# Kernel optimization log

Hardware: AMD Instinct MI355X
Metric: run time of the kernel (lower is better)

## Reference

```python
import jax, jax.numpy as jnp
import numpy as np
from jax import lax

B, T, V = 1024, 256, 64  # batch, time, num_classes (blank = V-1)
NEG = jnp.float32(-1e30)


def _greedy_decode(logits):
    """tf.nn.ctc_greedy_decoder: per-step argmax, merge repeated, drop blanks.
    Returns dense labels [B, T] (padded with blank) and lengths [B]."""
    blank = V - 1
    preds = jnp.argmax(logits, axis=-1).astype(jnp.int32)  # [B, T]
    prev = jnp.concatenate([jnp.full((B, 1), -1, jnp.int32), preds[:, :-1]], axis=1)
    keep = (preds != blank) & (preds != prev)  # merge_repeated=True
    pos = jnp.cumsum(keep, axis=1) - 1                      # target column for kept tokens
    col = jnp.where(keep, pos, T)                           # dump non-kept into scratch col T
    lab = jnp.full((B, T + 1), blank, jnp.int32)
    lab = lab.at[jnp.arange(B)[:, None], col].set(preds)[:, :T]
    length = jnp.sum(keep, axis=1).astype(jnp.int32)
    return lab, length


def _ctc_loss(logits, labels, lengths):
    """tf.nn.ctc_loss (blank_index=-1): log-space forward DP over extended labels."""
    blank = V - 1
    S = 2 * T + 1
    logp = jax.nn.log_softmax(logits)                       # [B, T, V]
    # extended label seq: blank, l1, blank, l2, ..., blank
    ext = jnp.full((B, S), blank, jnp.int32).at[:, 1::2].set(labels)
    ext_m2 = jnp.concatenate([jnp.full((B, 2), blank, jnp.int32), ext[:, :-2]], axis=1)
    allow_skip = (ext != blank) & (ext != ext_m2)           # [B, S]

    alpha0 = jnp.full((B, S), NEG, jnp.float32).at[:, 0].set(0.0)

    def step(alpha, logp_t):
        lp = jnp.take_along_axis(logp_t, ext, axis=1)       # [B, S]
        a2 = jnp.concatenate([jnp.full((B, 1), NEG), alpha[:, :-1]], axis=1)
        a3 = jnp.concatenate([jnp.full((B, 2), NEG), alpha[:, :-2]], axis=1)
        a3 = jnp.where(allow_skip, a3, NEG)
        new = jnp.logaddexp(jnp.logaddexp(alpha, a2), a3) + lp
        return new, None

    alpha, _ = lax.scan(step, alpha0, jnp.swapaxes(logp, 0, 1))  # scan over T
    end = 2 * lengths                                        # [B] index of final blank
    e1 = jnp.take_along_axis(alpha, end[:, None], axis=1)[:, 0]
    e2 = jnp.take_along_axis(alpha, jnp.maximum(end - 1, 0)[:, None], axis=1)[:, 0]
    e2 = jnp.where(lengths > 0, e2, NEG)
    return -jnp.logaddexp(e1, e2)


def setup_inputs() -> dict:
    key = jax.random.key(0)
    inputs = jax.random.normal(key, (B, T, V), dtype=jnp.float32)
    return {"inputs": inputs}


def reference(inputs):
    labels, lengths = _greedy_decode(inputs)
    loss = _ctc_loss(inputs, labels, lengths)
    probability = jnp.exp(-loss)
    # (decoded label ids stand in for the joined strings; lengths delimit them)
    return labels, lengths, probability
```

## Files before the change

kernel.cpp:

```cpp
#include <hip/hip_runtime.h>


#define BB 1024
#define TT 256
#define VV 64
#define BLANKC 63
#define K_LOG2E 1.44269504088896340736f

__global__ __launch_bounds__(256) void k1_decode(const float* __restrict__ logits,
                                                 float2* __restrict__ lsepb,
                                                 unsigned char* __restrict__ pred)
{
    const int gid = blockIdx.x * 256 + threadIdx.x;
    const float4* rp = (const float4*)(logits + (size_t)gid * VV);
    float4 v[16];
    #pragma unroll
    for (int i = 0; i < 16; ++i) v[i] = rp[i];

    float m = v[0].x; int idx = 0;
    #pragma unroll
    for (int i = 0; i < 16; ++i) {
        if (v[i].x > m) { m = v[i].x; idx = 4*i+0; }
        if (v[i].y > m) { m = v[i].y; idx = 4*i+1; }
        if (v[i].z > m) { m = v[i].z; idx = 4*i+2; }
        if (v[i].w > m) { m = v[i].w; idx = 4*i+3; }
    }
    float s0=0.f, s1=0.f, s2=0.f, s3=0.f;
    #pragma unroll
    for (int i = 0; i < 16; ++i) {
        s0 += exp2f((v[i].x - m) * K_LOG2E);
        s1 += exp2f((v[i].y - m) * K_LOG2E);
        s2 += exp2f((v[i].z - m) * K_LOG2E);
        s3 += exp2f((v[i].w - m) * K_LOG2E);
    }
    const float s = (s0 + s1) + (s2 + s3);
    const float lse2 = m * K_LOG2E + log2f(s);
    const float pb   = exp2f(fmaf(v[15].w, K_LOG2E, -lse2));
    lsepb[gid] = make_float2(lse2, pb);
    pred[gid]  = (unsigned char)idx;
}

#define STEP(XV, LS) { \
    const float lse2 = (LS).x, pbv = (LS).y; \
    const float q0 = exp2f(fmaf((XV)[0], K_LOG2E, -lse2)); \
    const float q1 = exp2f(fmaf((XV)[1], K_LOG2E, -lse2)); \
    const float q2 = exp2f(fmaf((XV)[2], K_LOG2E, -lse2)); \
    const float q3 = exp2f(fmaf((XV)[3], K_LOG2E, -lse2)); \
    float nb = __shfl_up(a7, 1, 64); nb = (lane == 0) ? 0.0f : nb; \
    const float na0 = (a0 + nb) * pbv; \
    const float na1 = (a1 + a0 + sk0 * nb) * q0; \
    const float na2 = (a2 + a1) * pbv; \
    const float na3 = (a3 + a2 + sk1 * a1) * q1; \
    const float na4 = (a4 + a3) * pbv; \
    const float na5 = (a5 + a4 + sk2 * a3) * q2; \
    const float na6 = (a6 + a5) * pbv; \
    const float na7 = (a7 + a6 + sk3 * a5) * q3; \
    a8 = (a8 + a7) * pbv; \
    a0 = na0; a1 = na1; a2 = na2; a3 = na3; \
    a4 = na4; a5 = na5; a6 = na6; a7 = na7; \
}

__global__ __launch_bounds__(64) void k2_dp(const float* __restrict__ logits,
                                            const float2* __restrict__ lsepb,
                                            const unsigned char* __restrict__ pred,
                                            float* __restrict__ out)
{
    __shared__ int    lab_s[TT];
    __shared__ float2 lsepb_s[TT];
    __shared__ float  alpha_s[520];

    const int lane = threadIdx.x;
    const int b    = blockIdx.x;

    {
        const float4* src = (const float4*)(lsepb + (size_t)b * TT);
        float4 u0 = src[2*lane], u1 = src[2*lane + 1];
        ((float4*)lsepb_s)[2*lane]     = u0;
        ((float4*)lsepb_s)[2*lane + 1] = u1;
    }

    uchar4 pc = ((const uchar4*)(pred + (size_t)b * TT))[lane];
    const int p0 = pc.x, p1 = pc.y, p2 = pc.z, p3 = pc.w;
    int pl = __shfl_up(p3, 1, 64); if (lane == 0) pl = -1;
    const int k0 = (p0 != BLANKC && p0 != pl);
    const int k1 = (p1 != BLANKC && p1 != p0);
    const int k2 = (p2 != BLANKC && p2 != p1);
    const int k3 = (p3 != BLANKC && p3 != p2);
    const int cnt = k0 + k1 + k2 + k3;
    int sc = cnt;
    #pragma unroll
    for (int off = 1; off < 64; off <<= 1) {
        int t = __shfl_up(sc, off, 64);
        if (lane >= off) sc += t;
    }
    const int length = __shfl(sc, 63, 64);
    int pos = sc - cnt;
    ((int4*)lab_s)[lane] = make_int4(BLANKC, BLANKC, BLANKC, BLANKC);
    if (k0) lab_s[pos++] = p0;
    if (k1) lab_s[pos++] = p1;
    if (k2) lab_s[pos++] = p2;
    if (k3) lab_s[pos++] = p3;

    const int4 lq = ((const int4*)lab_s)[lane];
    ((float4*)(out + (size_t)b * TT))[lane] =
        make_float4((float)lq.x, (float)lq.y, (float)lq.z, (float)lq.w);
    if (lane == 0) out[(size_t)BB * TT + b] = (float)length;

    int lprev = __shfl_up(lq.w, 1, 64); if (lane == 0) lprev = BLANKC;
    const float sk0 = (lq.x != BLANKC && lq.x != lprev) ? 1.0f : 0.0f;
    const float sk1 = (lq.y != BLANKC && lq.y != lq.x) ? 1.0f : 0.0f;
    const float sk2 = (lq.z != BLANKC && lq.z != lq.y) ? 1.0f : 0.0f;
    const float sk3 = (lq.w != BLANKC && lq.w != lq.z) ? 1.0f : 0.0f;
    const int vo0 = lq.x, vo1 = lq.y, vo2 = lq.z, vo3 = lq.w;

    float a0=0.f,a1=0.f,a2=0.f,a3=0.f,a4=0.f,a5=0.f,a6=0.f,a7=0.f,a8=0.f;
    if (lane == 0) a0 = 1.0f;
    int E = 0;

    const float* Lt = logits + (size_t)b * (TT * VV);
    float  xA[8][4], xB[8][4];
    float2 lsA[8],  lsB[8];

    #pragma unroll
    for (int u = 0; u < 8; ++u) {
        xA[u][0] = Lt[u*64 + vo0]; xA[u][1] = Lt[u*64 + vo1];
        xA[u][2] = Lt[u*64 + vo2]; xA[u][3] = Lt[u*64 + vo3];
        lsA[u] = lsepb_s[u];
    }

    #pragma unroll 1
    for (int tb = 0; tb < 16; ++tb) {
        const int t0 = tb * 16;
        #pragma unroll
        for (int u = 0; u < 8; ++u) {
            const int tt = 8 + u;
            xB[u][0] = Lt[tt*64 + vo0]; xB[u][1] = Lt[tt*64 + vo1];
            xB[u][2] = Lt[tt*64 + vo2]; xB[u][3] = Lt[tt*64 + vo3];
            lsB[u] = lsepb_s[t0 + 8 + u];
        }
        #pragma unroll
        for (int u = 0; u < 8; ++u) STEP(xA[u], lsA[u]);

        Lt += 1024;
        if (tb < 15) {
            #pragma unroll
            for (int u = 0; u < 8; ++u) {
                xA[u][0] = Lt[u*64 + vo0]; xA[u][1] = Lt[u*64 + vo1];
                xA[u][2] = Lt[u*64 + vo2]; xA[u][3] = Lt[u*64 + vo3];
                lsA[u] = lsepb_s[t0 + 16 + u];
            }
        }
        #pragma unroll
        for (int u = 0; u < 8; ++u) STEP(xB[u], lsB[u]);

        if (tb & 1) {
            float M = fmaxf(fmaxf(fmaxf(a0,a1), fmaxf(a2,a3)),
                            fmaxf(fmaxf(a4,a5), fmaxf(a6,a7)));
            M = fmaxf(M, a8);
            #pragma unroll
            for (int off = 1; off < 64; off <<= 1)
                M = fmaxf(M, __shfl_xor(M, off, 64));
            int e = (int)((__float_as_uint(M) >> 23) & 255) - 127;
            if (M == 0.0f) e = 0;
            const float scl = ldexpf(1.0f, -e);
            E += e;
            a0*=scl; a1*=scl; a2*=scl; a3*=scl; a4*=scl;
            a5*=scl; a6*=scl; a7*=scl; a8*=scl;
        }
    }

    ((float4*)alpha_s)[2*lane]     = make_float4(a0, a1, a2, a3);
    ((float4*)alpha_s)[2*lane + 1] = make_float4(a4, a5, a6, a7);
    if (lane == 63) alpha_s[512] = a8;
    if (lane == 0) {
        const int end = 2 * length;
        const float e1 = alpha_s[end];
        const float e2 = (length > 0) ? alpha_s[end - 1] : 0.0f;
        out[(size_t)BB * TT + BB + b] = exp2f(log2f(e1 + e2) + (float)E);
    }
}

extern "C" void kernel_launch(void* const* d_in, const int* in_sizes, int n_in,
                              void* d_out, int out_size, void* d_ws, size_t ws_size,
                              hipStream_t stream)
{
    const float* logits = (const float*)d_in[0];
    float* out = (float*)d_out;
    float2* lsepb = (float2*)d_ws;
    unsigned char* pred = (unsigned char*)d_ws + (size_t)2097152;
    hipLaunchKernelGGL(k1_decode, dim3(BB * TT / 256), dim3(256), 0, stream,
                       logits, lsepb, pred);
    hipLaunchKernelGGL(k2_dp, dim3(BB), dim3(64), 0, stream,
                       logits, lsepb, pred, out);
}
```

Baseline: 138.3 us.

## Fuse softmax/argmax decode and CTC DP into one kernel with LDS-staged probabilities

Measured after the change: 144.2 us. +4.2%, slower.

```diff
diff --git a/kernel.cpp b/kernel.cpp
--- a/kernel.cpp
+++ b/kernel.cpp
@@ -7,79 +7,91 @@
 #define BLANKC 63
 #define K_LOG2E 1.44269504088896340736f
 
-__global__ __launch_bounds__(256) void k1_decode(const float* __restrict__ logits,
-                                                 float2* __restrict__ lsepb,
-                                                 unsigned char* __restrict__ pred)
-{
-    const int gid = blockIdx.x * 256 + threadIdx.x;
-    const float4* rp = (const float4*)(logits + (size_t)gid * VV);
-    float4 v[16];
-    #pragma unroll
-    for (int i = 0; i < 16; ++i) v[i] = rp[i];
-
-    float m = v[0].x; int idx = 0;
-    #pragma unroll
-    for (int i = 0; i < 16; ++i) {
-        if (v[i].x > m) { m = v[i].x; idx = 4*i+0; }
-        if (v[i].y > m) { m = v[i].y; idx = 4*i+1; }
-        if (v[i].z > m) { m = v[i].z; idx = 4*i+2; }
-        if (v[i].w > m) { m = v[i].w; idx = 4*i+3; }
-    }
-    float s0=0.f, s1=0.f, s2=0.f, s3=0.f;
-    #pragma unroll
-    for (int i = 0; i < 16; ++i) {
-        s0 += exp2f((v[i].x - m) * K_LOG2E);
-        s1 += exp2f((v[i].y - m) * K_LOG2E);
-        s2 += exp2f((v[i].z - m) * K_LOG2E);
-        s3 += exp2f((v[i].w - m) * K_LOG2E);
-    }
-    const float s = (s0 + s1) + (s2 + s3);
-    const float lse2 = m * K_LOG2E + log2f(s);
-    const float pb   = exp2f(fmaf(v[15].w, K_LOG2E, -lse2));
-    lsepb[gid] = make_float2(lse2, pb);
-    pred[gid]  = (unsigned char)idx;
+__device__ __forceinline__ float wave_shr1(float v) {
+    return __int_as_float(__builtin_amdgcn_update_dpp(
+        0, __float_as_int(v), 0x138, 0xf, 0xf, false));
 }
 
-#define STEP(XV, LS) { \
-    const float lse2 = (LS).x, pbv = (LS).y; \
-    const float q0 = exp2f(fmaf((XV)[0], K_LOG2E, -lse2)); \
-    const float q1 = exp2f(fmaf((XV)[1], K_LOG2E, -lse2)); \
-    const float q2 = exp2f(fmaf((XV)[2], K_LOG2E, -lse2)); \
-    const float q3 = exp2f(fmaf((XV)[3], K_LOG2E, -lse2)); \
-    float nb = __shfl_up(a7, 1, 64); nb = (lane == 0) ? 0.0f : nb; \
-    const float na0 = (a0 + nb) * pbv; \
-    const float na1 = (a1 + a0 + sk0 * nb) * q0; \
-    const float na2 = (a2 + a1) * pbv; \
-    const float na3 = (a3 + a2 + sk1 * a1) * q1; \
-    const float na4 = (a4 + a3) * pbv; \
-    const float na5 = (a5 + a4 + sk2 * a3) * q2; \
-    const float na6 = (a6 + a5) * pbv; \
-    const float na7 = (a7 + a6 + sk3 * a5) * q3; \
-    a8 = (a8 + a7) * pbv; \
+#define STEP(Q0, Q1, Q2, Q3, PBV) { \
+    const float nb  = wave_shr1(a7); \
+    const float na0 = (a0 + nb) * (PBV); \
+    const float na1 = fmaf(sk0, nb, a1 + a0) * (Q0); \
+    const float na2 = (a2 + a1) * (PBV); \
+    const float na3 = fmaf(sk1, a1, a3 + a2) * (Q1); \
+    const float na4 = (a4 + a3) * (PBV); \
+    const float na5 = fmaf(sk2, a3, a5 + a4) * (Q2); \
+    const float na6 = (a6 + a5) * (PBV); \
+    const float na7 = fmaf(sk3, a5, a7 + a6) * (Q3); \
+    a8 = (a8 + a7) * (PBV); \
     a0 = na0; a1 = na1; a2 = na2; a3 = na3; \
     a4 = na4; a5 = na5; a6 = na6; a7 = na7; \
 }
 
-__global__ __launch_bounds__(64) void k2_dp(const float* __restrict__ logits,
-                                            const float2* __restrict__ lsepb,
-                                            const unsigned char* __restrict__ pred,
-                                            float* __restrict__ out)
+#define LOADB(D0, D1, D2, D3, DP, T0) { \
+    _Pragma("unroll") \
+    for (int u = 0; u < 8; ++u) { \
+        const int rbase = ((T0) + u) * 64; \
+        D0[u] = P_s[rbase + vo0]; \
+        D1[u] = P_s[rbase + vo1]; \
+        D2[u] = P_s[rbase + vo2]; \
+        D3[u] = P_s[rbase + vo3]; \
+        DP[u] = P_s[rbase + BLANKC]; \
+    } \
+}
+
+__global__ __launch_bounds__(256) void ctc_fused(const float* __restrict__ logits,
+                                                 float* __restrict__ out)
 {
-    __shared__ int    lab_s[TT];
-    __shared__ float2 lsepb_s[TT];
-    __shared__ float  alpha_s[520];
+    __shared__ float P_s[TT * VV];
+    __shared__ int   pred_s[TT];
+    __shared__ int   lab_s[TT];
+    __shared__ float alpha_s[520];
 
-    const int lane = threadIdx.x;
+    const int tid  = threadIdx.x;
+    const int lane = tid & 63;
+    const int w    = tid >> 6;
     const int b    = blockIdx.x;
+    const int g    = lane >> 4, li = lane & 15;
 
-    {
-        const float4* src = (const float4*)(lsepb + (size_t)b * TT);
-        float4 u0 = src[2*lane], u1 = src[2*lane + 1];
-        ((float4*)lsepb_s)[2*lane]     = u0;
-        ((float4*)lsepb_s)[2*lane + 1] = u1;
+    const float4* Lg4 = (const float4*)(logits + (size_t)b * (TT * VV));
+
+    float4 v[16];
+    #pragma unroll
+    for (int i = 0; i < 16; ++i) v[i] = Lg4[(w + 4 * i) * 64 + lane];
+
+    #pragma unroll
+    for (int i = 0; i < 16; ++i) {
+        const int r4 = w + 4 * i;
+        const float4 x = v[i];
+        float m = x.x; int idx = 0;
+        if (x.y > m) { m = x.y; idx = 1; }
+        if (x.z > m) { m = x.z; idx = 2; }
+        if (x.w > m) { m = x.w; idx = 3; }
+        idx += li * 4;
+        #pragma unroll
+        for (int o = 1; o < 16; o <<= 1) {
+            float om = __shfl_xor(m, o, 64);
+            int   oi = __shfl_xor(idx, o, 64);
+            if (om > m || (om == m && oi < idx)) { m = om; idx = oi; }
+        }
+        float e = exp2f((x.x - m) * K_LOG2E) + exp2f((x.y - m) * K_LOG2E)
+                + exp2f((x.z - m) * K_LOG2E) + exp2f((x.w - m) * K_LOG2E);
+        #pragma unroll
+        for (int o = 1; o < 16; o <<= 1) e += __shfl_xor(e, o, 64);
+        const float lse2 = m * K_LOG2E + log2f(e);
+
+        float4 pv;
+        pv.x = exp2f(fmaf(x.x, K_LOG2E, -lse2));
+        pv.y = exp2f(fmaf(x.y, K_LOG2E, -lse2));
+        pv.z = exp2f(fmaf(x.z, K_LOG2E, -lse2));
+        pv.w = exp2f(fmaf(x.w, K_LOG2E, -lse2));
+        ((float4*)&P_s[r4 * 256])[lane] = pv;
+        if (li == 15) pred_s[r4 * 4 + g] = idx;
     }
+    __syncthreads();
+    if (w != 0) return;
 
-    uchar4 pc = ((const uchar4*)(pred + (size_t)b * TT))[lane];
+    const int4 pc = ((const int4*)pred_s)[lane];
     const int p0 = pc.x, p1 = pc.y, p2 = pc.z, p3 = pc.w;
     int pl = __shfl_up(p3, 1, 64); if (lane == 0) pl = -1;
     const int k0 = (p0 != BLANKC && p0 != pl);
@@ -117,60 +129,36 @@
     if (lane == 0) a0 = 1.0f;
     int E = 0;
 
-    const float* Lt = logits + (size_t)b * (TT * VV);
-    float  xA[8][4], xB[8][4];
-    float2 lsA[8],  lsB[8];
+    float qA0[8], qA1[8], qA2[8], qA3[8], pA[8];
+    float qB0[8], qB1[8], qB2[8], qB3[8], pB[8];
 
-    #pragma unroll
-    for (int u = 0; u < 8; ++u) {
-        xA[u][0] = Lt[u*64 + vo0]; xA[u][1] = Lt[u*64 + vo1];
-        xA[u][2] = Lt[u*64 + vo2]; xA[u][3] = Lt[u*64 + vo3];
-        lsA[u] = lsepb_s[u];
+    LOADB(qA0, qA1, qA2, qA3, pA, 0);
+    #pragma unroll 1
+    for (int c = 0; c < 16; ++c) {
+        const int t0 = c * 16;
+        LOADB(qB0, qB1, qB2, qB3, pB, t0 + 8);
+        #pragma unroll
+        for (int u = 0; u < 8; ++u) STEP(qA0[u], qA1[u], qA2[u], qA3[u], pA[u]);
+        if (c < 15) LOADB(qA0, qA1, qA2, qA3, pA, t0 + 16);
+        #pragma unroll
+        for (int u = 0; u < 8; ++u) STEP(qB0[u], qB1[u], qB2[u], qB3[u], pB[u]);
+
+        float M = fmaxf(fmaxf(fmaxf(a0, a1), fmaxf(a2, a3)),
+                        fmaxf(fmaxf(a4, a5), fmaxf(a6, a7)));
+        M = fmaxf(M, a8);
+        #pragma unroll
+        for (int o = 1; o < 64; o <<= 1)
+            M = fmaxf(M, __shfl_xor(M, o, 64));
+        int e = (int)((__float_as_uint(M) >> 23) & 255) - 127;
+        if (M == 0.0f) e = 0;
+        E += e;
+        const float scl = __int_as_float((127 - e) << 23);
+        a0*=scl; a1*=scl; a2*=scl; a3*=scl; a4*=scl;
+        a5*=scl; a6*=scl; a7*=scl; a8*=scl;
     }
 
-    #pragma unroll 1
-    for (int tb = 0; tb < 16; ++tb) {
-        const int t0 = tb * 16;
-        #pragma unroll
-        for (int u = 0; u < 8; ++u) {
-            const int tt = 8 + u;
-            xB[u][0] = Lt[tt*64 + vo0]; xB[u][1] = Lt[tt*64 + vo1];
-            xB[u][2] = Lt[tt*64 + vo2]; xB[u][3] = Lt[tt*64 + vo3];
-            lsB[u] = lsepb_s[t0 + 8 + u];
-        }
-        #pragma unroll
-        for (int u = 0; u < 8; ++u) STEP(xA[u], lsA[u]);
-
-        Lt += 1024;
-        if (tb < 15) {
-            #pragma unroll
-            for (int u = 0; u < 8; ++u) {
-                xA[u][0] = Lt[u*64 + vo0]; xA[u][1] = Lt[u*64 + vo1];
-                xA[u][2] = Lt[u*64 + vo2]; xA[u][3] = Lt[u*64 + vo3];
-                lsA[u] = lsepb_s[t0 + 16 + u];
-            }
-        }
-        #pragma unroll
-        for (int u = 0; u < 8; ++u) STEP(xB[u], lsB[u]);
-
-        if (tb & 1) {
-            float M = fmaxf(fmaxf(fmaxf(a0,a1), fmaxf(a2,a3)),
-                            fmaxf(fmaxf(a4,a5), fmaxf(a6,a7)));
-            M = fmaxf(M, a8);
-            #pragma unroll
-            for (int off = 1; off < 64; off <<= 1)
-                M = fmaxf(M, __shfl_xor(M, off, 64));
-            int e = (int)((__float_as_uint(M) >> 23) & 255) - 127;
-            if (M == 0.0f) e = 0;
-            const float scl = ldexpf(1.0f, -e);
-            E += e;
-            a0*=scl; a1*=scl; a2*=scl; a3*=scl; a4*=scl;
-            a5*=scl; a6*=scl; a7*=scl; a8*=scl;
-        }
-    }
-
-    ((float4*)alpha_s)[2*lane]     = make_float4(a0, a1, a2, a3);
-    ((float4*)alpha_s)[2*lane + 1] = make_float4(a4, a5, a6, a7);
+    ((float4*)alpha_s)[2 * lane]     = make_float4(a0, a1, a2, a3);
+    ((float4*)alpha_s)[2 * lane + 1] = make_float4(a4, a5, a6, a7);
     if (lane == 63) alpha_s[512] = a8;
     if (lane == 0) {
         const int end = 2 * length;
@@ -186,10 +174,5 @@
 {
     const float* logits = (const float*)d_in[0];
     float* out = (float*)d_out;
-    float2* lsepb = (float2*)d_ws;
-    unsigned char* pred = (unsigned char*)d_ws + (size_t)2097152;
-    hipLaunchKernelGGL(k1_decode, dim3(BB * TT / 256), dim3(256), 0, stream,
-                       logits, lsepb, pred);
-    hipLaunchKernelGGL(k2_dp, dim3(BB), dim3(64), 0, stream,
-                       logits, lsepb, pred, out);
+    hipLaunchKernelGGL(ctc_fused, dim3(BB), dim3(256), 0, stream, logits, out);
 }
```
